# Kernel tuning notes

Hardware: AMD Instinct MI355X
Metric: run time of the kernel (lower is better)

The kernel has to match this reference:

```python
import jax, jax.numpy as jnp
import numpy as np

N_NODES = 100000  # total nodes (60k type-a + 40k type-b)
N_EDGES = 3200000


def spmm(rows, cols, vals, x):
    # y[r] = sum_e vals[e] * x[cols[e]] for edges with rows[e] == r  (COO SpMM)
    return jax.ops.segment_sum(vals[:, None] * x[cols], rows, num_segments=N_NODES)


def setup_inputs() -> dict:
    key = jax.random.key(0)
    ks = jax.random.split(key, 12)
    d_a, d_b, n_hid, n_out = 256, 128, 256, 64
    s = lambda d: (1.0 / np.sqrt(d)).astype(np.float32)
    return {
        "x_a": jax.random.normal(ks[0], (60000, d_a), dtype=jnp.float32),
        "x_b": jax.random.normal(ks[1], (40000, d_b), dtype=jnp.float32),
        "rows": jax.random.randint(ks[2], (N_EDGES,), 0, N_NODES, dtype=jnp.int32),
        "cols": jax.random.randint(ks[3], (N_EDGES,), 0, N_NODES, dtype=jnp.int32),
        "vals": jax.random.uniform(ks[4], (N_EDGES,), dtype=jnp.float32),
        "W1a": jax.random.normal(ks[5], (d_a, n_hid), dtype=jnp.float32) * s(d_a),
        "b1a": jnp.zeros((n_hid,), dtype=jnp.float32),
        "W1b": jax.random.normal(ks[6], (d_b, n_hid), dtype=jnp.float32) * s(d_b),
        "b1b": jnp.zeros((n_hid,), dtype=jnp.float32),
        "Wf": jax.random.normal(ks[7], (n_hid, n_hid), dtype=jnp.float32) * s(n_hid),
        "bf": jnp.zeros((n_hid,), dtype=jnp.float32),
        "W2": jax.random.normal(ks[8], (n_hid, n_out), dtype=jnp.float32) * s(n_hid),
        "b2": jnp.zeros((n_out,), dtype=jnp.float32),
    }


def reference(x_a, x_b, rows, cols, vals, W1a, b1a, W1b, b1b, Wf, bf, W2, b2):
    # per-type Linear + ReLU (dropout p=0 -> identity in eval/reference)
    h_a = jax.nn.relu(x_a @ W1a + b1a)  # [60000, n_hid]
    h_b = jax.nn.relu(x_b @ W1b + b1b)  # [40000, n_hid]
    x = jnp.concatenate([h_a, h_b], axis=0)  # [N_NODES, n_hid]
    # hop - 1 = 1 intermediate hop: Linear -> SpMM -> ReLU
    x = x @ Wf + bf
    x = spmm(rows, cols, vals, x)
    x = jax.nn.relu(x)
    # output projection then final SpMM aggregation
    x = x @ W2 + b2
    x = spmm(rows, cols, vals, x)  # [N_NODES, n_out]
    return x
```

## Files before the change

### kernel.cpp

```cpp
#include <hip/hip_runtime.h>

#define NN 100000
#define NE 3200000
#define NA 60000
#define NB 40000
#define NHID 256
#define NOUT 64

#define RPB 64
#define NBUCK 1563
#define PBLK 256
#define CHUNK 12500

typedef unsigned short u16;
typedef unsigned int u32;
typedef __attribute__((ext_vector_type(8))) short short8;
typedef __attribute__((ext_vector_type(4))) float f32x4;

__device__ __forceinline__ float bf2f(u16 u) {
  return __uint_as_float(((u32)u) << 16);
}
__device__ __forceinline__ u16 f2bf(float f) {
  u32 u = __float_as_uint(f);
  u32 r = (u + 0x7fffu + ((u >> 16) & 1u)) >> 16;
  return (u16)r;
}
__device__ __forceinline__ float i8f(u32 dw, int b) {
  return (float)((int)(dw << (24 - 8 * b)) >> 24);
}

__device__ __forceinline__ void gload_lds16(const void* gsrc, void* ldst) {
  __builtin_amdgcn_global_load_lds(
      (const __attribute__((address_space(1))) void*)gsrc,
      (__attribute__((address_space(3))) void*)ldst, 16, 0, 0);
}

template <int BN, int RELU_OUT, int QUANT>
__global__ __launch_bounds__(256) void gemm_mfma(
    const u16* __restrict__ A, const u16* __restrict__ Bt,
    const float* __restrict__ bias, void* __restrict__ Cout,
    float* __restrict__ scales, int M, int N, int K) {
  constexpr int BM = 128;
  constexpr int FI = (BN == 128) ? 4 : 2;
  constexpr int WROWS = FI * 16;
  __shared__ __align__(16) u16 As[BM * 32];
  __shared__ __align__(16) u16 Bs[BN * 32];

  const int tid = threadIdx.x;
  const int w = tid >> 6;
  const int lane = tid & 63;
  const int bm = blockIdx.x * BM;
  const int bn = blockIdx.y * BN;
  const int wr = (BN == 128) ? (w >> 1) : w;
  const int wc = (BN == 128) ? (w & 1) : 0;

  f32x4 acc[FI][4];
#pragma unroll
  for (int i = 0; i < FI; ++i)
#pragma unroll
    for (int j = 0; j < 4; ++j) acc[i][j] = (f32x4)0.f;

  for (int k0 = 0; k0 < K; k0 += 32) {
#pragma unroll
    for (int s = 0; s < 2; ++s) {
      const int inst = w * 2 + s;
      const int row = inst * 16 + (lane >> 2);
      int rg = bm + row;
      if (rg > M - 1) rg = M - 1;
      const int c = (lane & 3) ^ ((row >> 1) & 3);
      gload_lds16(A + (size_t)rg * K + k0 + c * 8, &As[inst * 512]);
    }
    if (BN == 128) {
#pragma unroll
      for (int s = 0; s < 2; ++s) {
        const int inst = w * 2 + s;
        const int row = inst * 16 + (lane >> 2);
        const int c = (lane & 3) ^ ((row >> 1) & 3);
        gload_lds16(Bt + (size_t)(bn + row) * K + k0 + c * 8,
                    &Bs[inst * 512]);
      }
    } else {
      const int inst = w;
      const int row = inst * 16 + (lane >> 2);
      const int c = (lane & 3) ^ ((row >> 1) & 3);
      gload_lds16(Bt + (size_t)(bn + row) * K + k0 + c * 8, &Bs[inst * 512]);
    }
    __syncthreads();

    const int kc = lane >> 4;
    short8 af[FI], bfr[4];
#pragma unroll
    for (int i = 0; i < FI; ++i) {
      const int row = wr * WROWS + i * 16 + (lane & 15);
      const int ch = kc ^ ((row >> 1) & 3);
      af[i] = *reinterpret_cast<const short8*>(&As[row * 32 + ch * 8]);
    }
#pragma unroll
    for (int j = 0; j < 4; ++j) {
      const int row = wc * 64 + j * 16 + (lane & 15);
      const int ch = kc ^ ((row >> 1) & 3);
      bfr[j] = *reinterpret_cast<const short8*>(&Bs[row * 32 + ch * 8]);
    }
#pragma unroll
    for (int i = 0; i < FI; ++i)
#pragma unroll
      for (int j = 0; j < 4; ++j)
        acc[i][j] = __builtin_amdgcn_mfma_f32_16x16x32_bf16(af[i], bfr[j],
                                                            acc[i][j], 0, 0, 0);
    __syncthreads();
  }

  if constexpr (QUANT) {
    float bv[4];
#pragma unroll
    for (int j = 0; j < 4; ++j)
      bv[j] = bias[bn + wc * 64 + j * 16 + (lane & 15)];
    const int g = (bn >> 6) + wc;
    u32* zq = (u32*)Cout;
#pragma unroll
    for (int i = 0; i < FI; ++i) {
#pragma unroll
      for (int r = 0; r < 4; ++r) {
        float o[4];
#pragma unroll
        for (int j = 0; j < 4; ++j) o[j] = acc[i][j][r] + bv[j];
        float am = fmaxf(fmaxf(fabsf(o[0]), fabsf(o[1])),
                         fmaxf(fabsf(o[2]), fabsf(o[3])));
#pragma unroll
        for (int mk = 1; mk < 16; mk <<= 1) am = fmaxf(am, __shfl_xor(am, mk));
        const float sinv = am > 0.f ? 127.f / am : 0.f;
        const float sc = am > 0.f ? am / 127.f : 0.f;
        const int q0 = __float2int_rn(o[0] * sinv);
        const int q1 = __float2int_rn(o[1] * sinv);
        const int q2 = __float2int_rn(o[2] * sinv);
        const int q3 = __float2int_rn(o[3] * sinv);
        const u32 dw = (q0 & 0xff) | ((q1 & 0xff) << 8) | ((q2 & 0xff) << 16) |
                       ((q3 & 0xff) << 24);
        const int row = bm + wr * WROWS + i * 16 + (lane >> 4) * 4 + r;
        if (row < M) {
          zq[(size_t)row * 64 + g * 16 + (lane & 15)] = dw;
          if ((lane & 15) == 0) scales[(size_t)row * 4 + g] = sc;
        }
      }
    }
  } else {
    u16* C = (u16*)Cout;
#pragma unroll
    for (int i = 0; i < FI; ++i) {
#pragma unroll
      for (int j = 0; j < 4; ++j) {
        const int col = bn + wc * 64 + j * 16 + (lane & 15);
        const float bv = bias[col];
#pragma unroll
        for (int r = 0; r < 4; ++r) {
          const int row = bm + wr * WROWS + i * 16 + (lane >> 4) * 4 + r;
          if (row < M) {
            float o = acc[i][j][r] + bv;
            if (RELU_OUT) o = fmaxf(o, 0.f);
            C[(size_t)row * N + col] = f2bf(o);
          }
        }
      }
    }
  }
}

__global__ __launch_bounds__(256) void cvt_bf16(const float4* __restrict__ in,
                                                ushort4* __restrict__ out,
                                                int n4) {
  const int i = blockIdx.x * 256 + threadIdx.x;
  if (i >= n4) return;
  const float4 v = in[i];
  ushort4 o;
  o.x = f2bf(v.x); o.y = f2bf(v.y); o.z = f2bf(v.z); o.w = f2bf(v.w);
  out[i] = o;
}

__global__ __launch_bounds__(256) void wt_all(
    const float* __restrict__ W1a, const float* __restrict__ W1b,
    const float* __restrict__ Wf, const float* __restrict__ W2,
    u16* __restrict__ W1at, u16* __restrict__ W1bt, u16* __restrict__ Wft,
    u16* __restrict__ W2t) {
  const int i = blockIdx.x * 256 + threadIdx.x;
  if (i < 65536) {
    const int n = i >> 8, k = i & 255;
    W1at[i] = f2bf(W1a[k * 256 + n]);
  } else if (i < 98304) {
    const int t = i - 65536;
    const int n = t >> 7, k = t & 127;
    W1bt[t] = f2bf(W1b[k * 256 + n]);
  } else if (i < 163840) {
    const int t = i - 98304;
    const int n = t >> 8, k = t & 255;
    Wft[t] = f2bf(Wf[k * 256 + n]);
  } else if (i < 180224) {
    const int t = i - 163840;
    const int n = t >> 8, p = t & 255;
    const int f = ((p >> 6) << 6) + ((p & 3) << 4) + ((p >> 2) & 15);
    W2t[t] = f2bf(W2[f * 64 + n]);
  }
}

__global__ __launch_bounds__(256) void p1_hist(const int* __restrict__ rows,
                                               int* __restrict__ cnt) {
  __shared__ int h[NBUCK];
  const int tid = threadIdx.x;
  for (int i = tid; i < NBUCK; i += 256) h[i] = 0;
  __syncthreads();
  const int s = blockIdx.x * CHUNK;
  const int e = s + CHUNK;
  for (int i = s + tid; i < e; i += 256) atomicAdd(&h[rows[i] >> 6], 1);
  __syncthreads();
  for (int i = tid; i < NBUCK; i += 256) cnt[i * PBLK + blockIdx.x] = h[i];
}

__global__ __launch_bounds__(256) void s1_scan_blocks(int* __restrict__ cnt,
                                                      int* __restrict__ btot) {
  __shared__ int lds[256];
  const int bu = blockIdx.x;
  const int t = threadIdx.x;
  const int v = cnt[bu * PBLK + t];
  lds[t] = v;
  __syncthreads();
#pragma unroll
  for (int off = 1; off < 256; off <<= 1) {
    const int x = (t >= off) ? lds[t - off] : 0;
    __syncthreads();
    lds[t] += x;
    __syncthreads();
  }
  cnt[bu * PBLK + t] = lds[t] - v;
  if (t == 255) btot[bu] = lds[255];
}

__global__ __launch_bounds__(1024) void s2_scan_buckets(
    const int* __restrict__ btot, int* __restrict__ bstart) {
  __shared__ int lds[1024];
  __shared__ int carry;
  const int t = threadIdx.x;
  if (t == 0) carry = 0;
  __syncthreads();
  for (int base = 0; base < NBUCK; base += 1024) {
    const int i = base + t;
    const int v = (i < NBUCK) ? btot[i] : 0;
    lds[t] = v;
    __syncthreads();
#pragma unroll
    for (int off = 1; off < 1024; off <<= 1) {
      const int x = (t >= off) ? lds[t - off] : 0;
      __syncthreads();
      lds[t] += x;
      __syncthreads();
    }
    const int excl = lds[t] - v;
    const int c = carry;
    if (i < NBUCK) bstart[i] = c + excl;
    __syncthreads();
    if (t == 0) carry = c + lds[1023];
    __syncthreads();
  }
  if (t == 0) bstart[NBUCK] = NE;
}

__global__ __launch_bounds__(256) void p3_scatter(
    const int* __restrict__ rows, const int* __restrict__ cols,
    const float* __restrict__ vals, const int* __restrict__ cnt,
    const int* __restrict__ bstart, int2* __restrict__ edges) {
  __shared__ int lcur[NBUCK];
  const int tid = threadIdx.x;
  const int blk = blockIdx.x;
  for (int bu = tid; bu < NBUCK; bu += 256)
    lcur[bu] = bstart[bu] + cnt[bu * PBLK + blk];
  __syncthreads();
  const int s = blk * CHUNK;
  const int e = s + CHUNK;
  for (int i = s + tid; i < e; i += 256) {
    const int r = rows[i];
    const int bu = r >> 6;
    const int lr = r & 63;
    const int pos = atomicAdd(&lcur[bu], 1);
    edges[pos] = make_int2(cols[i] | (lr << 17), __float_as_int(vals[i]));
  }
}

__global__ __launch_bounds__(256) void sort_bucket(
    const int* __restrict__ bstart, const int2* __restrict__ edges,
    int2* __restrict__ edges2, int* __restrict__ rptr) {
  __shared__ int hist[RPB];
  __shared__ int sc[RPB];
  __shared__ int cur[RPB];
  const int bu = blockIdx.x;
  const int t = threadIdx.x;
  const int s = bstart[bu], e = bstart[bu + 1];
  if (t < RPB) hist[t] = 0;
  __syncthreads();
  for (int i = s + t; i < e; i += 256)
    atomicAdd(&hist[(edges[i].x >> 17) & 63], 1);
  __syncthreads();
  const int hv = (t < RPB) ? hist[t] : 0;
  if (t < RPB) sc[t] = hv;
  __syncthreads();
#pragma unroll
  for (int off = 1; off < RPB; off <<= 1) {
    const int x = (t >= off && t < RPB) ? sc[t - off] : 0;
    __syncthreads();
    if (t < RPB) sc[t] += x;
    __syncthreads();
  }
  if (t < RPB) {
    const int base = s + sc[t] - hv;
    cur[t] = base;
    const int grow = bu * RPB + t;
    if (grow < NN) rptr[grow] = base;
  }
  if (bu == 0 && t == 0) rptr[NN] = NE;
  __syncthreads();
  for (int i = s + t; i < e; i += 256) {
    const int2 ed = edges[i];
    const int lr = (ed.x >> 17) & 63;
    const int pos = atomicAdd(&cur[lr], 1);
    edges2[pos] = make_int2(ed.x & 0x1FFFF, ed.y);
  }
}

__global__ __launch_bounds__(256) void spmm256_q8(
    const int* __restrict__ ptr, const int2* __restrict__ edges,
    const u32* __restrict__ Zq, const float* __restrict__ scales,
    u16* __restrict__ Yb) {
  const int wid = (int)((blockIdx.x * (size_t)256 + threadIdx.x) >> 6);
  const int lane = threadIdx.x & 63;
  if (wid >= NN) return;
  const int s = ptr[wid], e = ptr[wid + 1];
  const int gsel = lane >> 4;
  float a0 = 0.f, a1 = 0.f, a2 = 0.f, a3 = 0.f;
  int j = s;
  for (; j + 7 < e; j += 8) {
    int2 ed[8];
#pragma unroll
    for (int q = 0; q < 8; ++q) ed[q] = edges[j + q];
    u32 dw[8];
    float sc[8];
#pragma unroll
    for (int q = 0; q < 8; ++q) {
      dw[q] = Zq[(size_t)ed[q].x * 64 + lane];
      sc[q] = scales[(size_t)ed[q].x * 4 + gsel];
    }
#pragma unroll
    for (int q = 0; q < 8; ++q) {
      const float vs = __int_as_float(ed[q].y) * sc[q];
      a0 += vs * i8f(dw[q], 0);
      a1 += vs * i8f(dw[q], 1);
      a2 += vs * i8f(dw[q], 2);
      a3 += vs * i8f(dw[q], 3);
    }
  }
  for (; j < e; ++j) {
    const int2 e0 = edges[j];
    const u32 dw = Zq[(size_t)e0.x * 64 + lane];
    const float vs =
        __int_as_float(e0.y) * scales[(size_t)e0.x * 4 + gsel];
    a0 += vs * i8f(dw, 0);
    a1 += vs * i8f(dw, 1);
    a2 += vs * i8f(dw, 2);
    a3 += vs * i8f(dw, 3);
  }
  ushort4 o;
  o.x = f2bf(fmaxf(a0, 0.f));
  o.y = f2bf(fmaxf(a1, 0.f));
  o.z = f2bf(fmaxf(a2, 0.f));
  o.w = f2bf(fmaxf(a3, 0.f));
  reinterpret_cast<ushort4*>(Yb + (size_t)wid * 256)[lane] = o;
}

__global__ __launch_bounds__(256) void spmm64_csr(
    const int* __restrict__ ptr, const int2* __restrict__ edges,
    const u16* __restrict__ Zb, float* __restrict__ Y) {
  const int wid = (int)((blockIdx.x * (size_t)256 + threadIdx.x) >> 6);
  const int lane = threadIdx.x & 63;
  if (wid >= NN) return;
  const int s = ptr[wid], e = ptr[wid + 1];
  float acc = 0.f;
  int j = s;
  for (; j + 7 < e; j += 8) {
    int2 ed[8];
#pragma unroll
    for (int q = 0; q < 8; ++q) ed[q] = edges[j + q];
    u16 u[8];
#pragma unroll
    for (int q = 0; q < 8; ++q) u[q] = Zb[(size_t)ed[q].x * 64 + lane];
#pragma unroll
    for (int q = 0; q < 8; ++q)
      acc += __int_as_float(ed[q].y) * bf2f(u[q]);
  }
  for (; j < e; ++j)
    acc += __int_as_float(edges[j].y) * bf2f(Zb[(size_t)edges[j].x * 64 + lane]);
  Y[(size_t)wid * 64 + lane] = acc;
}

extern "C" void kernel_launch(void* const* d_in, const int* in_sizes, int n_in,
                              void* d_out, int out_size, void* d_ws,
                              size_t ws_size, hipStream_t stream) {
  const float* x_a  = (const float*)d_in[0];
  const float* x_b  = (const float*)d_in[1];
  const int*   rows = (const int*)d_in[2];
  const int*   cols = (const int*)d_in[3];
  const float* vals = (const float*)d_in[4];
  const float* W1a  = (const float*)d_in[5];
  const float* b1a  = (const float*)d_in[6];
  const float* W1b  = (const float*)d_in[7];
  const float* b1b  = (const float*)d_in[8];
  const float* Wf   = (const float*)d_in[9];
  const float* bf   = (const float*)d_in[10];
  const float* W2   = (const float*)d_in[11];
  const float* b2   = (const float*)d_in[12];
  float* out = (float*)d_out;

  char* p = (char*)d_ws;
  u16* h    = (u16*)p;  p += (size_t)NN * NHID * 2;
  u32* zq   = (u32*)p;  p += (size_t)NN * 64 * 4;
  float* zscale = (float*)p; p += (size_t)NN * 4 * 4;
  u16* z2b  = (u16*)p;  p += (size_t)NN * NOUT * 2;
  u16* xab  = (u16*)p;  p += (size_t)NA * 256 * 2;
  u16* xbb  = (u16*)p;  p += (size_t)NB * 128 * 2;
  u16* W1at = (u16*)p;  p += 256 * 256 * 2;
  u16* W1bt = (u16*)p;  p += 256 * 128 * 2;
  u16* Wft  = (u16*)p;  p += 256 * 256 * 2;
  u16* W2t  = (u16*)p;  p += 64 * 256 * 2;
  int2* edges = (int2*)p; p += (size_t)NE * 8;
  int* cnt    = (int*)p;  p += (size_t)NBUCK * PBLK * 4;
  int* btot   = (int*)p;  p += (size_t)((NBUCK + 3) & ~3) * 4;
  int* bstart = (int*)p;  p += (size_t)((NBUCK + 4) & ~3) * 4;
  int* rptr   = (int*)p;  p += (size_t)(NN + 4) * 4;
  u16* s1b = h;
  int2* edges2 = (int2*)xab;

  cvt_bf16<<<(NA * 256 / 4 + 255) / 256, 256, 0, stream>>>(
      (const float4*)x_a, (ushort4*)xab, NA * 256 / 4);
  cvt_bf16<<<(NB * 128 / 4 + 255) / 256, 256, 0, stream>>>(
      (const float4*)x_b, (ushort4*)xbb, NB * 128 / 4);
  wt_all<<<704, 256, 0, stream>>>(W1a, W1b, Wf, W2, W1at, W1bt, Wft, W2t);

  gemm_mfma<128, 1, 0><<<dim3((NA + 127) / 128, 2), 256, 0, stream>>>(
      xab, W1at, b1a, h, nullptr, NA, NHID, 256);
  gemm_mfma<128, 1, 0><<<dim3((NB + 127) / 128, 2), 256, 0, stream>>>(
      xbb, W1bt, b1b, h + (size_t)NA * NHID, nullptr, NB, NHID, 128);
  gemm_mfma<128, 0, 1><<<dim3((NN + 127) / 128, 2), 256, 0, stream>>>(
      h, Wft, bf, zq, zscale, NN, NHID, 256);

  p1_hist<<<PBLK, 256, 0, stream>>>(rows, cnt);
  s1_scan_blocks<<<NBUCK, 256, 0, stream>>>(cnt, btot);
  s2_scan_buckets<<<1, 1024, 0, stream>>>(btot, bstart);
  p3_scatter<<<PBLK, 256, 0, stream>>>(rows, cols, vals, cnt, bstart, edges);
  sort_bucket<<<NBUCK, 256, 0, stream>>>(bstart, edges, edges2, rptr);

  spmm256_q8<<<(NN * 64 + 255) / 256, 256, 0, stream>>>(rptr, edges2, zq,
                                                        zscale, s1b);
  gemm_mfma<64, 0, 0><<<dim3((NN + 127) / 128, 1), 256, 0, stream>>>(
      s1b, W2t, b2, z2b, nullptr, NN, NOUT, 256);
  spmm64_csr<<<(NN * 64 + 255) / 256, 256, 0, stream>>>(rptr, edges2, z2b, out);
}
```

Measured before the change: 501.7 us.

## Quantize output projection to int8 and buffer bucket edges in LDS

The second SpMM now gathers int8-quantized rows with one scale per row, replacing bf16 rows, which halves the bytes gathered per edge. The bucketing pass uses half as many partition blocks with twice the threads each, and sort_bucket stages each bucket's edges in shared memory when they fit, so it reads global memory once instead of twice. In exchange the final output is less precise because it goes through int8 quantization.

Result: slower. 529.5 us (+5.5%).

```diff
diff --git a/kernel.cpp b/kernel.cpp
--- a/kernel.cpp
+++ b/kernel.cpp
@@ -9,8 +9,9 @@
 
 #define RPB 64
 #define NBUCK 1563
-#define PBLK 256
-#define CHUNK 12500
+#define PBLK 128
+#define CHUNK 25000
+#define SCAP 3072
 
 typedef unsigned short u16;
 typedef unsigned int u32;
@@ -110,7 +111,7 @@
     __syncthreads();
   }
 
-  if constexpr (QUANT) {
+  if constexpr (QUANT == 1) {
     float bv[4];
 #pragma unroll
     for (int j = 0; j < 4; ++j)
@@ -129,7 +130,7 @@
 #pragma unroll
         for (int mk = 1; mk < 16; mk <<= 1) am = fmaxf(am, __shfl_xor(am, mk));
         const float sinv = am > 0.f ? 127.f / am : 0.f;
-        const float sc = am > 0.f ? am / 127.f : 0.f;
+        const float scv = am > 0.f ? am / 127.f : 0.f;
         const int q0 = __float2int_rn(o[0] * sinv);
         const int q1 = __float2int_rn(o[1] * sinv);
         const int q2 = __float2int_rn(o[2] * sinv);
@@ -139,7 +140,38 @@
         const int row = bm + wr * WROWS + i * 16 + (lane >> 4) * 4 + r;
         if (row < M) {
           zq[(size_t)row * 64 + g * 16 + (lane & 15)] = dw;
-          if ((lane & 15) == 0) scales[(size_t)row * 4 + g] = sc;
+          if ((lane & 15) == 0) scales[(size_t)row * 4 + g] = scv;
+        }
+      }
+    }
+  } else if constexpr (QUANT == 2) {
+    float bv[4];
+#pragma unroll
+    for (int j = 0; j < 4; ++j) bv[j] = bias[j * 16 + (lane & 15)];
+    u32* zq = (u32*)Cout;
+#pragma unroll
+    for (int i = 0; i < FI; ++i) {
+#pragma unroll
+      for (int r = 0; r < 4; ++r) {
+        float o[4];
+#pragma unroll
+        for (int j = 0; j < 4; ++j) o[j] = acc[i][j][r] + bv[j];
+        float am = fmaxf(fmaxf(fabsf(o[0]), fabsf(o[1])),
+                         fmaxf(fabsf(o[2]), fabsf(o[3])));
+#pragma unroll
+        for (int mk = 1; mk < 16; mk <<= 1) am = fmaxf(am, __shfl_xor(am, mk));
+        const float sinv = am > 0.f ? 127.f / am : 0.f;
+        const float scv = am > 0.f ? am / 127.f : 0.f;
+        const int q0 = __float2int_rn(o[0] * sinv);
+        const int q1 = __float2int_rn(o[1] * sinv);
+        const int q2 = __float2int_rn(o[2] * sinv);
+        const int q3 = __float2int_rn(o[3] * sinv);
+        const u32 dw = (q0 & 0xff) | ((q1 & 0xff) << 8) | ((q2 & 0xff) << 16) |
+                       ((q3 & 0xff) << 24);
+        const int row = bm + wr * WROWS + i * 16 + (lane >> 4) * 4 + r;
+        if (row < M) {
+          zq[(size_t)row * 16 + (lane & 15)] = dw;
+          if ((lane & 15) == 0) scales[row] = scv;
         }
       }
     }
@@ -214,23 +246,23 @@
   for (int i = tid; i < NBUCK; i += 256) cnt[i * PBLK + blockIdx.x] = h[i];
 }
 
-__global__ __launch_bounds__(256) void s1_scan_blocks(int* __restrict__ cnt,
-                                                      int* __restrict__ btot) {
-  __shared__ int lds[256];
+__global__ __launch_bounds__(PBLK) void s1_scan_blocks(int* __restrict__ cnt,
+                                                       int* __restrict__ btot) {
+  __shared__ int lds[PBLK];
   const int bu = blockIdx.x;
   const int t = threadIdx.x;
   const int v = cnt[bu * PBLK + t];
   lds[t] = v;
   __syncthreads();
 #pragma unroll
-  for (int off = 1; off < 256; off <<= 1) {
+  for (int off = 1; off < PBLK; off <<= 1) {
     const int x = (t >= off) ? lds[t - off] : 0;
     __syncthreads();
     lds[t] += x;
     __syncthreads();
   }
   cnt[bu * PBLK + t] = lds[t] - v;
-  if (t == 255) btot[bu] = lds[255];
+  if (t == PBLK - 1) btot[bu] = lds[PBLK - 1];
 }
 
 __global__ __launch_bounds__(1024) void s2_scan_buckets(
@@ -262,19 +294,19 @@
   if (t == 0) bstart[NBUCK] = NE;
 }
 
-__global__ __launch_bounds__(256) void p3_scatter(
+__global__ __launch_bounds__(512) void p3_scatter(
     const int* __restrict__ rows, const int* __restrict__ cols,
     const float* __restrict__ vals, const int* __restrict__ cnt,
     const int* __restrict__ bstart, int2* __restrict__ edges) {
   __shared__ int lcur[NBUCK];
   const int tid = threadIdx.x;
   const int blk = blockIdx.x;
-  for (int bu = tid; bu < NBUCK; bu += 256)
+  for (int bu = tid; bu < NBUCK; bu += 512)
     lcur[bu] = bstart[bu] + cnt[bu * PBLK + blk];
   __syncthreads();
   const int s = blk * CHUNK;
   const int e = s + CHUNK;
-  for (int i = s + tid; i < e; i += 256) {
+  for (int i = s + tid; i < e; i += 512) {
     const int r = rows[i];
     const int bu = r >> 6;
     const int lr = r & 63;
@@ -286,16 +318,27 @@
 __global__ __launch_bounds__(256) void sort_bucket(
     const int* __restrict__ bstart, const int2* __restrict__ edges,
     int2* __restrict__ edges2, int* __restrict__ rptr) {
+  __shared__ int2 ebuf[SCAP];
   __shared__ int hist[RPB];
   __shared__ int sc[RPB];
   __shared__ int cur[RPB];
   const int bu = blockIdx.x;
   const int t = threadIdx.x;
   const int s = bstart[bu], e = bstart[bu + 1];
+  const int n = e - s;
+  const bool useL = (n <= SCAP);
   if (t < RPB) hist[t] = 0;
-  __syncthreads();
-  for (int i = s + t; i < e; i += 256)
-    atomicAdd(&hist[(edges[i].x >> 17) & 63], 1);
+  if (useL) {
+    for (int i = t; i < n; i += 256) ebuf[i] = edges[s + i];
+  }
+  __syncthreads();
+  if (useL) {
+    for (int i = t; i < n; i += 256)
+      atomicAdd(&hist[(ebuf[i].x >> 17) & 63], 1);
+  } else {
+    for (int i = s + t; i < e; i += 256)
+      atomicAdd(&hist[(edges[i].x >> 17) & 63], 1);
+  }
   __syncthreads();
   const int hv = (t < RPB) ? hist[t] : 0;
   if (t < RPB) sc[t] = hv;
@@ -315,11 +358,20 @@
   }
   if (bu == 0 && t == 0) rptr[NN] = NE;
   __syncthreads();
-  for (int i = s + t; i < e; i += 256) {
-    const int2 ed = edges[i];
-    const int lr = (ed.x >> 17) & 63;
-    const int pos = atomicAdd(&cur[lr], 1);
-    edges2[pos] = make_int2(ed.x & 0x1FFFF, ed.y);
+  if (useL) {
+    for (int i = t; i < n; i += 256) {
+      const int2 ed = ebuf[i];
+      const int lr = (ed.x >> 17) & 63;
+      const int pos = atomicAdd(&cur[lr], 1);
+      edges2[pos] = make_int2(ed.x & 0x1FFFF, ed.y);
+    }
+  } else {
+    for (int i = s + t; i < e; i += 256) {
+      const int2 ed = edges[i];
+      const int lr = (ed.x >> 17) & 63;
+      const int pos = atomicAdd(&cur[lr], 1);
+      edges2[pos] = make_int2(ed.x & 0x1FFFF, ed.y);
+    }
   }
 }
 
@@ -372,28 +424,38 @@
   reinterpret_cast<ushort4*>(Yb + (size_t)wid * 256)[lane] = o;
 }
 
-__global__ __launch_bounds__(256) void spmm64_csr(
+__global__ __launch_bounds__(256) void spmm64_q8(
     const int* __restrict__ ptr, const int2* __restrict__ edges,
-    const u16* __restrict__ Zb, float* __restrict__ Y) {
+    const u32* __restrict__ Z2q, const float* __restrict__ zsc2,
+    float* __restrict__ Y) {
   const int wid = (int)((blockIdx.x * (size_t)256 + threadIdx.x) >> 6);
   const int lane = threadIdx.x & 63;
   if (wid >= NN) return;
   const int s = ptr[wid], e = ptr[wid + 1];
+  const int dwi = lane & 15;
+  const int byi = lane >> 4;
   float acc = 0.f;
   int j = s;
   for (; j + 7 < e; j += 8) {
     int2 ed[8];
 #pragma unroll
     for (int q = 0; q < 8; ++q) ed[q] = edges[j + q];
-    u16 u[8];
-#pragma unroll
-    for (int q = 0; q < 8; ++q) u[q] = Zb[(size_t)ed[q].x * 64 + lane];
+    u32 dw[8];
+    float sc[8];
+#pragma unroll
+    for (int q = 0; q < 8; ++q) {
+      dw[q] = Z2q[(size_t)ed[q].x * 16 + dwi];
+      sc[q] = zsc2[ed[q].x];
+    }
 #pragma unroll
     for (int q = 0; q < 8; ++q)
-      acc += __int_as_float(ed[q].y) * bf2f(u[q]);
-  }
-  for (; j < e; ++j)
-    acc += __int_as_float(edges[j].y) * bf2f(Zb[(size_t)edges[j].x * 64 + lane]);
+      acc += __int_as_float(ed[q].y) * sc[q] * i8f(dw[q], byi);
+  }
+  for (; j < e; ++j) {
+    const int2 e0 = edges[j];
+    const u32 dw = Z2q[(size_t)e0.x * 16 + dwi];
+    acc += __int_as_float(e0.y) * zsc2[e0.x] * i8f(dw, byi);
+  }
   Y[(size_t)wid * 64 + lane] = acc;
 }
 
@@ -419,7 +481,8 @@
   u16* h    = (u16*)p;  p += (size_t)NN * NHID * 2;
   u32* zq   = (u32*)p;  p += (size_t)NN * 64 * 4;
   float* zscale = (float*)p; p += (size_t)NN * 4 * 4;
-  u16* z2b  = (u16*)p;  p += (size_t)NN * NOUT * 2;
+  u32* z2q  = (u32*)p;  p += (size_t)NN * 16 * 4;
+  float* zsc2 = (float*)p; p += (size_t)NN * 4;
   u16* xab  = (u16*)p;  p += (size_t)NA * 256 * 2;
   u16* xbb  = (u16*)p;  p += (size_t)NB * 128 * 2;
   u16* W1at = (u16*)p;  p += 256 * 256 * 2;
@@ -448,14 +511,15 @@
       h, Wft, bf, zq, zscale, NN, NHID, 256);
 
   p1_hist<<<PBLK, 256, 0, stream>>>(rows, cnt);
-  s1_scan_blocks<<<NBUCK, 256, 0, stream>>>(cnt, btot);
+  s1_scan_blocks<<<NBUCK, PBLK, 0, stream>>>(cnt, btot);
   s2_scan_buckets<<<1, 1024, 0, stream>>>(btot, bstart);
-  p3_scatter<<<PBLK, 256, 0, stream>>>(rows, cols, vals, cnt, bstart, edges);
+  p3_scatter<<<PBLK, 512, 0, stream>>>(rows, cols, vals, cnt, bstart, edges);
   sort_bucket<<<NBUCK, 256, 0, stream>>>(bstart, edges, edges2, rptr);
 
   spmm256_q8<<<(NN * 64 + 255) / 256, 256, 0, stream>>>(rptr, edges2, zq,
                                                         zscale, s1b);
-  gemm_mfma<64, 0, 0><<<dim3((NN + 127) / 128, 1), 256, 0, stream>>>(
-      s1b, W2t, b2, z2b, nullptr, NN, NOUT, 256);
-  spmm64_csr<<<(NN * 64 + 255) / 256, 256, 0, stream>>>(rptr, edges2, z2b, out);
-}
+  gemm_mfma<64, 0, 2><<<dim3((NN + 127) / 128, 1), 256, 0, stream>>>(
+      s1b, W2t, b2, z2q, zsc2, NN, NOUT, 256);
+  spmm64_q8<<<(NN * 64 + 255) / 256, 256, 0, stream>>>(rptr, edges2, z2q,
+                                                       zsc2, out);
+}
```
